# Kernel tuning notes

Measured on AMD Instinct MI355X. Metric: run time of the kernel, lower is better.

## Reference

```python
import jax, jax.numpy as jnp
import numpy as np

B, T, D, H = 131072, 30, 10, 20
EPS = 1e-5


def setup_inputs() -> dict:
    key = jax.random.key(0)
    ks = jax.random.split(key, 8)
    rn = lambda k, s: (jax.random.normal(k, s, dtype=jnp.float32) * 0.1)
    return {
        "x": jax.random.normal(ks[0], (B, T, D), dtype=jnp.float32),
        "g0": jnp.ones((T, 2 * D), jnp.float32),
        "be0": jnp.zeros((T, 2 * D), jnp.float32),
        "W1": rn(ks[1], (T, H, 2 * D)),
        "b1": rn(ks[2], (T, H)),
        "g1": jnp.ones((T, H), jnp.float32),
        "be1": jnp.zeros((T, H), jnp.float32),
        "W2": rn(ks[3], (T, H, H)),
        "b2": rn(ks[4], (T, H)),
        "g2": jnp.ones((T, H), jnp.float32),
        "be2": jnp.zeros((T, H), jnp.float32),
        "W3": rn(ks[5], (T, D, H)),
        "b3": rn(ks[6], (T, D)),
    }


def _bn(x, g, b):
    # training-mode BatchNorm1d: batch stats, biased variance, eps=1e-5
    mu = x.mean(0)
    var = ((x - mu) ** 2).mean(0)
    return (x - mu) * jax.lax.rsqrt(var + EPS) * g + b


def _forward(x, g0, be0, W1, b1, g1, be1, W2, b2, g2, be2, W3, b3):
    xs = jnp.swapaxes(x, 0, 1)  # [T, B, D] time-major

    def step(prev, ps):
        xt, g0t, be0t, W1t, b1t, g1t, be1t, W2t, b2t, g2t, be2t, W3t, b3t = ps
        h = jnp.concatenate([xt, prev], axis=1)      # [B, 2D] recurrent concat
        h = _bn(h, g0t, be0t)
        h = jax.nn.relu(_bn(h @ W1t.T + b1t, g1t, be1t))  # [B, H]
        h = jax.nn.relu(_bn(h @ W2t.T + b2t, g2t, be2t))  # [B, H]
        out = h @ W3t.T + b3t                              # [B, D]
        return out, out

    init = jnp.zeros((x.shape[0], D), dtype=x.dtype)
    _, outs = jax.lax.scan(step, init, (xs, g0, be0, W1, b1, g1, be1, W2, b2, g2, be2, W3, b3))
    return jnp.swapaxes(outs, 0, 1)  # [B, T, D]


def reference(x, g0, be0, W1, b1, g1, be1, W2, b2, g2, be2, W3, b3):
    return _forward(x, g0, be0, W1, b1, g1, be1, W2, b2, g2, be2, W3, b3)
```

## Files before the change

### kernel.cpp

```cpp
#include <hip/hip_runtime.h>

static constexpr int   BATCH = 131072;
static constexpr int   TS    = 30;
static constexpr int   DD    = 10;
static constexpr int   HH    = 20;
static constexpr float EPSV  = 1e-5f;
static constexpr float INV_B = 1.0f / (float)BATCH;

static constexpr int NBLK = 256;
static constexpr int NTHR = 256;
static constexpr int RPT  = 2;
static constexpr int TT   = NBLK * NTHR;
static constexpr int NS   = 8;
static constexpr int GRPS = 8;
static constexpr int GSZ  = NBLK / GRPS;
static constexpr int NVA  = 230;
static constexpr int NVB  = 40;
static constexpr int STRA = NVA * NS;
static constexpr int STRB = NVB * NS;
static constexpr int CTRW = 160;

__device__ __forceinline__ int tri(int k, int l) {
    return k * (41 - k) / 2 + (l - k);
}

template <int CTRL>
__device__ __forceinline__ float dpp_add(float v) {
    int x = __builtin_amdgcn_update_dpp(0, __float_as_int(v), CTRL, 0xF, 0xF, true);
    return v + __int_as_float(x);
}

__device__ __forceinline__ float rowsum16(float v) {
    v = dpp_add<0x111>(v);
    v = dpp_add<0x112>(v);
    v = dpp_add<0x114>(v);
    v = dpp_add<0x118>(v);
    return v;
}

__device__ __forceinline__ float aloadf(const float* p) {
    return __hip_atomic_load(p, __ATOMIC_RELAXED, __HIP_MEMORY_SCOPE_AGENT);
}

__device__ __forceinline__ void gbar(unsigned* __restrict__ base, int tid, int grp8) {
    __syncthreads();
    if (tid == 0) {
        if (__hip_atomic_fetch_add(base + grp8 * 16, 1u, __ATOMIC_RELAXED,
                                   __HIP_MEMORY_SCOPE_AGENT) == (unsigned)(GSZ - 1))
            __hip_atomic_fetch_add(base + 128, 1u, __ATOMIC_RELAXED,
                                   __HIP_MEMORY_SCOPE_AGENT);
        while (__hip_atomic_load(base + 128, __ATOMIC_RELAXED,
                                 __HIP_MEMORY_SCOPE_AGENT) < (unsigned)GRPS)
            __builtin_amdgcn_s_sleep(1);
    }
    __syncthreads();
}

__global__ void __launch_bounds__(NTHR)
k_init(const float* __restrict__ x, float* __restrict__ prevg, float* __restrict__ redA)
{
    __shared__ float lred[16 * NVA];
    const int tid     = threadIdx.x;
    const int grp     = tid >> 4;
    const bool lane15 = (tid & 15) == 15;
    const int gt      = blockIdx.x * NTHR + tid;

    float xv[RPT][DD];
#pragma unroll
    for (int r = 0; r < RPT; ++r) {
        const float2* px = reinterpret_cast<const float2*>(x + (size_t)(gt + r * TT) * TS * DD);
#pragma unroll
        for (int i = 0; i < 5; ++i) { float2 v = px[i]; xv[r][2 * i] = v.x; xv[r][2 * i + 1] = v.y; }
    }
#pragma unroll
    for (int r = 0; r < RPT; ++r)
#pragma unroll
        for (int d = 0; d < DD; ++d) prevg[(size_t)d * BATCH + gt + r * TT] = 0.0f;

#define H0A(i) ((i) < DD ? xv[0][i] : 0.0f)
#define H0B(i) ((i) < DD ? xv[1][i] : 0.0f)
    {
        int v = 0;
#pragma unroll
        for (int k = 0; k < 2 * DD; ++k) {
#pragma unroll
            for (int l = k; l < 2 * DD; ++l) {
                float p = fmaf(H0A(k), H0A(l), H0B(k) * H0B(l));
                float r = rowsum16(p);
                if (lane15) lred[grp * NVA + v] = r;
                ++v;
            }
        }
#pragma unroll
        for (int k = 0; k < 2 * DD; ++k) {
            float r = rowsum16(H0A(k) + H0B(k));
            if (lane15) lred[grp * NVA + 210 + k] = r;
        }
    }
#undef H0A
#undef H0B
    __syncthreads();
    if (tid < NVA) {
        float acc = 0.0f;
#pragma unroll
        for (int g = 0; g < 16; ++g) acc += lred[g * NVA + tid];
        atomicAdd(redA + tid * NS + (blockIdx.x & (NS - 1)), acc);
    }
}

template <bool LAST>
__global__ void __launch_bounds__(NTHR)
k_step(const float* __restrict__ x, float* __restrict__ prevg, float* __restrict__ outg,
       const float* __restrict__ W1, const float* __restrict__ W2,
       const float* __restrict__ W3, const float* __restrict__ b3,
       const float* __restrict__ g0, const float* __restrict__ be0,
       const float* __restrict__ g1, const float* __restrict__ be1,
       const float* __restrict__ g2, const float* __restrict__ be2,
       float* __restrict__ redA, float* __restrict__ redB,
       unsigned* __restrict__ ctr, int t)
{
    __shared__ float lred[16 * NVA];
    __shared__ float sM[230], sMu[20], sCov[400], sU[400], sP[400];
    __shared__ float sW1[400], sW2[400], sW3[200], sB3[10];
    __shared__ float sA0[20], sC0[20], sA1[20], sC1[20], sA2[20], sC2[20];

    const int tid     = threadIdx.x;
    const int grp     = tid >> 4;
    const bool lane15 = (tid & 15) == 15;
    const int slot    = blockIdx.x & (NS - 1);
    const int grp8    = blockIdx.x & (GRPS - 1);
    const int gt      = blockIdx.x * NTHR + tid;

    float xv[RPT][DD], pv[RPT][DD], xn[RPT][DD];
#pragma unroll
    for (int r = 0; r < RPT; ++r) {
        const float2* px = reinterpret_cast<const float2*>(x + (size_t)(gt + r * TT) * TS * DD + t * DD);
#pragma unroll
        for (int i = 0; i < 5; ++i) { float2 v = px[i]; xv[r][2 * i] = v.x; xv[r][2 * i + 1] = v.y; }
    }
#pragma unroll
    for (int r = 0; r < RPT; ++r)
#pragma unroll
        for (int d = 0; d < DD; ++d) pv[r][d] = prevg[(size_t)d * BATCH + gt + r * TT];
    if constexpr (!LAST) {
#pragma unroll
        for (int r = 0; r < RPT; ++r) {
            const float2* px = reinterpret_cast<const float2*>(x + (size_t)(gt + r * TT) * TS * DD + (t + 1) * DD);
#pragma unroll
            for (int i = 0; i < 5; ++i) { float2 v = px[i]; xn[r][2 * i] = v.x; xn[r][2 * i + 1] = v.y; }
        }
    }

    for (int i = tid; i < 400; i += NTHR) { sW1[i] = W1[t * 400 + i]; sW2[i] = W2[t * 400 + i]; }
    if (tid < 200) sW3[tid] = W3[t * 200 + tid];
    if (tid >= 200 && tid < 210) sB3[tid - 200] = b3[t * DD + (tid - 200)];

    if (tid < NVA) {
        const float* p = redA + (size_t)t * STRA + tid * NS;
        float s = 0.0f;
#pragma unroll
        for (int i = 0; i < NS; ++i) s += p[i];
        sM[tid] = s;
    }
    __syncthreads();

    if (tid < 20) {
        float mu  = sM[210 + tid] * INV_B;
        float var = fmaf(-mu, mu, sM[tri(tid, tid)] * INV_B);
        float a   = g0[t * 20 + tid] * rsqrtf(var + EPSV);
        sA0[tid] = a;
        sC0[tid] = fmaf(-mu, a, be0[t * 20 + tid]);
        sMu[tid] = mu;
    }
    __syncthreads();

    for (int i = tid; i < 400; i += NTHR) {
        int k = i / 20, l = i % 20;
        int a = k < l ? k : l, b = k < l ? l : k;
        sCov[i] = fmaf(-sMu[k], sMu[l], sM[tri(a, b)] * INV_B);
        sU[i]   = sW1[i] * sA0[l];
    }
    __syncthreads();

    for (int i = tid; i < 400; i += NTHR) {
        int j = i / 20, k = i % 20;
        float acc = 0.0f;
#pragma unroll
        for (int l = 0; l < 20; ++l)
            acc = fmaf(sCov[k * 20 + l], sU[j * 20 + l], acc);
        sP[i] = acc * sU[i];
    }
    __syncthreads();

    if (tid < 20) {
        float var1 = 0.0f, m1 = 0.0f;
#pragma unroll
        for (int k = 0; k < 20; ++k) {
            var1 += sP[tid * 20 + k];
            m1    = fmaf(sU[tid * 20 + k], sMu[k], m1);
            m1    = fmaf(sW1[tid * 20 + k], sC0[k], m1);
        }
        float a1 = g1[t * 20 + tid] * rsqrtf(var1 + EPSV);
        sA1[tid] = a1;
        sC1[tid] = fmaf(-m1, a1, be1[t * 20 + tid]);
    }
    __syncthreads();

    float y2[RPT][HH];
#pragma unroll
    for (int r = 0; r < RPT; ++r) {
        float hn[20];
#pragma unroll
        for (int k = 0; k < 10; ++k) hn[k]      = fmaf(xv[r][k], sA0[k],      sC0[k]);
#pragma unroll
        for (int k = 0; k < 10; ++k) hn[10 + k] = fmaf(pv[r][k], sA0[10 + k], sC0[10 + k]);

        float h1[20];
#pragma unroll
        for (int j = 0; j < 20; ++j) {
            float y = 0.0f;
#pragma unroll
            for (int k = 0; k < 20; ++k) y = fmaf(sW1[j * 20 + k], hn[k], y);
            h1[j] = fmaxf(fmaf(y, sA1[j], sC1[j]), 0.0f);
        }
#pragma unroll
        for (int j = 0; j < 20; ++j) {
            float y = 0.0f;
#pragma unroll
            for (int k = 0; k < 20; ++k) y = fmaf(sW2[j * 20 + k], h1[k], y);
            y2[r][j] = y;
        }
    }

#pragma unroll
    for (int j = 0; j < 20; ++j) {
        float r = rowsum16(y2[0][j] + y2[1][j]);
        if (lane15) lred[grp * NVA + j] = r;
    }
#pragma unroll
    for (int j = 0; j < 20; ++j) {
        float r = rowsum16(fmaf(y2[0][j], y2[0][j], y2[1][j] * y2[1][j]));
        if (lane15) lred[grp * NVA + 20 + j] = r;
    }
    __syncthreads();
    if (tid < NVB) {
        float acc = 0.0f;
#pragma unroll
        for (int g = 0; g < 16; ++g) acc += lred[g * NVA + tid];
        atomicAdd(redB + (size_t)t * STRB + tid * NS + slot, acc);
    }

    gbar(ctr + (size_t)t * CTRW, tid, grp8);

    if (tid < NVB) {
        const float* p = redB + (size_t)t * STRB + tid * NS;
        float s = 0.0f;
#pragma unroll
        for (int i = 0; i < NS; ++i) s += aloadf(p + i);
        sM[tid] = s;
    }
    __syncthreads();
    if (tid < 20) {
        float m   = sM[tid] * INV_B;
        float var = fmaf(-m, m, sM[20 + tid] * INV_B);
        float a   = g2[t * 20 + tid] * rsqrtf(var + EPSV);
        sA2[tid] = a;
        sC2[tid] = fmaf(-m, a, be2[t * 20 + tid]);
    }
    __syncthreads();

    float ov[RPT][DD];
#pragma unroll
    for (int r = 0; r < RPT; ++r) {
        float h2[20];
#pragma unroll
        for (int j = 0; j < 20; ++j)
            h2[j] = fmaxf(fmaf(y2[r][j], sA2[j], sC2[j]), 0.0f);
#pragma unroll
        for (int d = 0; d < DD; ++d) {
            float a = sB3[d];
#pragma unroll
            for (int j = 0; j < 20; ++j)
                a = fmaf(sW3[d * 20 + j], h2[j], a);
            ov[r][d] = a;
        }
        float2* po = reinterpret_cast<float2*>(outg + (size_t)(gt + r * TT) * TS * DD + t * DD);
#pragma unroll
        for (int i = 0; i < 5; ++i) po[i] = make_float2(ov[r][2 * i], ov[r][2 * i + 1]);
#pragma unroll
        for (int d = 0; d < DD; ++d) prevg[(size_t)d * BATCH + gt + r * TT] = ov[r][d];
    }

    if constexpr (!LAST) {
#define H0A(i) ((i) < DD ? xn[0][i] : ov[0][(i) - DD])
#define H0B(i) ((i) < DD ? xn[1][i] : ov[1][(i) - DD])
        {
            int v = 0;
#pragma unroll
            for (int k = 0; k < 2 * DD; ++k) {
#pragma unroll
                for (int l = k; l < 2 * DD; ++l) {
                    float p = fmaf(H0A(k), H0A(l), H0B(k) * H0B(l));
                    float r = rowsum16(p);
                    if (lane15) lred[grp * NVA + v] = r;
                    ++v;
                }
            }
#pragma unroll
            for (int k = 0; k < 2 * DD; ++k) {
                float r = rowsum16(H0A(k) + H0B(k));
                if (lane15) lred[grp * NVA + 210 + k] = r;
            }
        }
#undef H0A
#undef H0B
        __syncthreads();
        if (tid < NVA) {
            float acc = 0.0f;
#pragma unroll
            for (int g = 0; g < 16; ++g) acc += lred[g * NVA + tid];
            atomicAdd(redA + (size_t)(t + 1) * STRA + tid * NS + slot, acc);
        }
    }
}

extern "C" void kernel_launch(void* const* d_in, const int* in_sizes, int n_in,
                              void* d_out, int out_size, void* d_ws, size_t ws_size,
                              hipStream_t stream) {
    const float* x   = (const float*)d_in[0];
    const float* g0  = (const float*)d_in[1];
    const float* be0 = (const float*)d_in[2];
    const float* W1  = (const float*)d_in[3];
    const float* b1  = (const float*)d_in[4];   (void)b1;
    const float* g1  = (const float*)d_in[5];
    const float* be1 = (const float*)d_in[6];
    const float* W2  = (const float*)d_in[7];
    const float* b2  = (const float*)d_in[8];   (void)b2;
    const float* g2  = (const float*)d_in[9];
    const float* be2 = (const float*)d_in[10];
    const float* W3  = (const float*)d_in[11];
    const float* b3  = (const float*)d_in[12];
    float* out = (float*)d_out;

    const size_t redA_f = (size_t)TS * STRA;
    const size_t redB_f = (size_t)TS * STRB;
    const size_t ctr_u  = (size_t)TS * CTRW;
    float*    redA  = (float*)d_ws;
    float*    redB  = redA + redA_f;
    unsigned* ctr   = (unsigned*)(redB + redB_f);
    float*    prevg = (float*)(ctr + ctr_u);

    hipMemsetAsync(d_ws, 0, (redA_f + redB_f) * 4 + ctr_u * 4, stream);

    k_init<<<NBLK, NTHR, 0, stream>>>(x, prevg, redA);

    for (int t = 0; t < TS; ++t) {
        if (t + 1 < TS)
            k_step<false><<<NBLK, NTHR, 0, stream>>>(x, prevg, out, W1, W2, W3, b3,
                                                     g0, be0, g1, be1, g2, be2,
                                                     redA, redB, ctr, t);
        else
            k_step<true><<<NBLK, NTHR, 0, stream>>>(x, prevg, out, W1, W2, W3, b3,
                                                    g0, be0, g1, be1, g2, be2,
                                                    redA, redB, ctr, t);
    }
}
```

Measured before the change: 1.338 ms.

## Fuse all timesteps into one persistent kernel with grid barriers

Replaces the init kernel plus thirty per-step launches with a single persistent kernel that loops over timesteps. Software grid barriers on per-phase counters stand in for kernel boundaries. The recurrent state now stays in registers instead of round-tripping through a global prevg buffer. This removes launch gaps and global traffic for the state, but relies on all 256 blocks being co-resident and adds spin-wait barrier latency.

```diff
diff --git a/kernel.cpp b/kernel.cpp
--- a/kernel.cpp
+++ b/kernel.cpp
@@ -19,6 +19,7 @@
 static constexpr int STRA = NVA * NS;
 static constexpr int STRB = NVB * NS;
 static constexpr int CTRW = 160;
+static constexpr int NPH  = 2 * TS + 1;
 
 __device__ __forceinline__ int tri(int k, int l) {
     return k * (41 - k) / 2 + (l - k);
@@ -57,67 +58,14 @@
 }
 
 __global__ void __launch_bounds__(NTHR)
-k_init(const float* __restrict__ x, float* __restrict__ prevg, float* __restrict__ redA)
-{
-    __shared__ float lred[16 * NVA];
-    const int tid     = threadIdx.x;
-    const int grp     = tid >> 4;
-    const bool lane15 = (tid & 15) == 15;
-    const int gt      = blockIdx.x * NTHR + tid;
-
-    float xv[RPT][DD];
-#pragma unroll
-    for (int r = 0; r < RPT; ++r) {
-        const float2* px = reinterpret_cast<const float2*>(x + (size_t)(gt + r * TT) * TS * DD);
-#pragma unroll
-        for (int i = 0; i < 5; ++i) { float2 v = px[i]; xv[r][2 * i] = v.x; xv[r][2 * i + 1] = v.y; }
-    }
-#pragma unroll
-    for (int r = 0; r < RPT; ++r)
-#pragma unroll
-        for (int d = 0; d < DD; ++d) prevg[(size_t)d * BATCH + gt + r * TT] = 0.0f;
-
-#define H0A(i) ((i) < DD ? xv[0][i] : 0.0f)
-#define H0B(i) ((i) < DD ? xv[1][i] : 0.0f)
-    {
-        int v = 0;
-#pragma unroll
-        for (int k = 0; k < 2 * DD; ++k) {
-#pragma unroll
-            for (int l = k; l < 2 * DD; ++l) {
-                float p = fmaf(H0A(k), H0A(l), H0B(k) * H0B(l));
-                float r = rowsum16(p);
-                if (lane15) lred[grp * NVA + v] = r;
-                ++v;
-            }
-        }
-#pragma unroll
-        for (int k = 0; k < 2 * DD; ++k) {
-            float r = rowsum16(H0A(k) + H0B(k));
-            if (lane15) lred[grp * NVA + 210 + k] = r;
-        }
-    }
-#undef H0A
-#undef H0B
-    __syncthreads();
-    if (tid < NVA) {
-        float acc = 0.0f;
-#pragma unroll
-        for (int g = 0; g < 16; ++g) acc += lred[g * NVA + tid];
-        atomicAdd(redA + tid * NS + (blockIdx.x & (NS - 1)), acc);
-    }
-}
-
-template <bool LAST>
-__global__ void __launch_bounds__(NTHR)
-k_step(const float* __restrict__ x, float* __restrict__ prevg, float* __restrict__ outg,
-       const float* __restrict__ W1, const float* __restrict__ W2,
-       const float* __restrict__ W3, const float* __restrict__ b3,
-       const float* __restrict__ g0, const float* __restrict__ be0,
-       const float* __restrict__ g1, const float* __restrict__ be1,
-       const float* __restrict__ g2, const float* __restrict__ be2,
-       float* __restrict__ redA, float* __restrict__ redB,
-       unsigned* __restrict__ ctr, int t)
+rnn_all(const float* __restrict__ x, float* __restrict__ outg,
+        const float* __restrict__ W1, const float* __restrict__ W2,
+        const float* __restrict__ W3, const float* __restrict__ b3,
+        const float* __restrict__ g0, const float* __restrict__ be0,
+        const float* __restrict__ g1, const float* __restrict__ be1,
+        const float* __restrict__ g2, const float* __restrict__ be2,
+        float* __restrict__ redA, float* __restrict__ redB,
+        unsigned* __restrict__ ctr)
 {
     __shared__ float lred[16 * NVA];
     __shared__ float sM[230], sMu[20], sCov[400], sU[400], sP[400];
@@ -131,195 +79,238 @@
     const int grp8    = blockIdx.x & (GRPS - 1);
     const int gt      = blockIdx.x * NTHR + tid;
 
-    float xv[RPT][DD], pv[RPT][DD], xn[RPT][DD];
+    float pv[RPT][DD];
+#pragma unroll
+    for (int r = 0; r < RPT; ++r)
+#pragma unroll
+        for (int d = 0; d < DD; ++d) pv[r][d] = 0.0f;
+
+    float xv[RPT][DD];
 #pragma unroll
     for (int r = 0; r < RPT; ++r) {
-        const float2* px = reinterpret_cast<const float2*>(x + (size_t)(gt + r * TT) * TS * DD + t * DD);
+        const float2* px = reinterpret_cast<const float2*>(x + (size_t)(gt + r * TT) * TS * DD);
 #pragma unroll
         for (int i = 0; i < 5; ++i) { float2 v = px[i]; xv[r][2 * i] = v.x; xv[r][2 * i + 1] = v.y; }
     }
-#pragma unroll
-    for (int r = 0; r < RPT; ++r)
-#pragma unroll
-        for (int d = 0; d < DD; ++d) pv[r][d] = prevg[(size_t)d * BATCH + gt + r * TT];
-    if constexpr (!LAST) {
+
+#define H0A(i) ((i) < DD ? xv[0][i] : 0.0f)
+#define H0B(i) ((i) < DD ? xv[1][i] : 0.0f)
+    {
+        int v = 0;
+#pragma unroll
+        for (int k = 0; k < 2 * DD; ++k) {
+#pragma unroll
+            for (int l = k; l < 2 * DD; ++l) {
+                float p = fmaf(H0A(k), H0A(l), H0B(k) * H0B(l));
+                float r = rowsum16(p);
+                if (lane15) lred[grp * NVA + v] = r;
+                ++v;
+            }
+        }
+#pragma unroll
+        for (int k = 0; k < 2 * DD; ++k) {
+            float r = rowsum16(H0A(k) + H0B(k));
+            if (lane15) lred[grp * NVA + 210 + k] = r;
+        }
+    }
+#undef H0A
+#undef H0B
+    __syncthreads();
+    if (tid < NVA) {
+        float acc = 0.0f;
+#pragma unroll
+        for (int g = 0; g < 16; ++g) acc += lred[g * NVA + tid];
+        atomicAdd(redA + tid * NS + slot, acc);
+    }
+    gbar(ctr + (size_t)(2 * TS) * CTRW, tid, grp8);
+
+    for (int t = 0; t < TS; ++t) {
+        for (int i = tid; i < 400; i += NTHR) { sW1[i] = W1[t * 400 + i]; sW2[i] = W2[t * 400 + i]; }
+        if (tid < 200) sW3[tid] = W3[t * 200 + tid];
+        if (tid >= 200 && tid < 210) sB3[tid - 200] = b3[t * DD + (tid - 200)];
+
+        float xn[RPT][DD];
+        if (t + 1 < TS) {
+#pragma unroll
+            for (int r = 0; r < RPT; ++r) {
+                const float2* px = reinterpret_cast<const float2*>(x + (size_t)(gt + r * TT) * TS * DD + (t + 1) * DD);
+#pragma unroll
+                for (int i = 0; i < 5; ++i) { float2 v = px[i]; xn[r][2 * i] = v.x; xn[r][2 * i + 1] = v.y; }
+            }
+        }
+
+        if (tid < NVA) {
+            const float* p = redA + (size_t)t * STRA + tid * NS;
+            float s = 0.0f;
+#pragma unroll
+            for (int i = 0; i < NS; ++i) s += aloadf(p + i);
+            sM[tid] = s;
+        }
+        __syncthreads();
+
+        if (tid < 20) {
+            float mu  = sM[210 + tid] * INV_B;
+            float var = fmaf(-mu, mu, sM[tri(tid, tid)] * INV_B);
+            float a   = g0[t * 20 + tid] * rsqrtf(var + EPSV);
+            sA0[tid] = a;
+            sC0[tid] = fmaf(-mu, a, be0[t * 20 + tid]);
+            sMu[tid] = mu;
+        }
+        __syncthreads();
+
+        for (int i = tid; i < 400; i += NTHR) {
+            int k = i / 20, l = i % 20;
+            int a = k < l ? k : l, b = k < l ? l : k;
+            sCov[i] = fmaf(-sMu[k], sMu[l], sM[tri(a, b)] * INV_B);
+            sU[i]   = sW1[i] * sA0[l];
+        }
+        __syncthreads();
+
+        for (int i = tid; i < 400; i += NTHR) {
+            int j = i / 20, k = i % 20;
+            float acc = 0.0f;
+#pragma unroll
+            for (int l = 0; l < 20; ++l)
+                acc = fmaf(sCov[k * 20 + l], sU[j * 20 + l], acc);
+            sP[i] = acc * sU[i];
+        }
+        __syncthreads();
+
+        if (tid < 20) {
+            float var1 = 0.0f, m1 = 0.0f;
+#pragma unroll
+            for (int k = 0; k < 20; ++k) {
+                var1 += sP[tid * 20 + k];
+                m1    = fmaf(sU[tid * 20 + k], sMu[k], m1);
+                m1    = fmaf(sW1[tid * 20 + k], sC0[k], m1);
+            }
+            float a1 = g1[t * 20 + tid] * rsqrtf(var1 + EPSV);
+            sA1[tid] = a1;
+            sC1[tid] = fmaf(-m1, a1, be1[t * 20 + tid]);
+        }
+        __syncthreads();
+
+        float y2[RPT][HH];
 #pragma unroll
         for (int r = 0; r < RPT; ++r) {
-            const float2* px = reinterpret_cast<const float2*>(x + (size_t)(gt + r * TT) * TS * DD + (t + 1) * DD);
-#pragma unroll
-            for (int i = 0; i < 5; ++i) { float2 v = px[i]; xn[r][2 * i] = v.x; xn[r][2 * i + 1] = v.y; }
-        }
-    }
-
-    for (int i = tid; i < 400; i += NTHR) { sW1[i] = W1[t * 400 + i]; sW2[i] = W2[t * 400 + i]; }
-    if (tid < 200) sW3[tid] = W3[t * 200 + tid];
-    if (tid >= 200 && tid < 210) sB3[tid - 200] = b3[t * DD + (tid - 200)];
-
-    if (tid < NVA) {
-        const float* p = redA + (size_t)t * STRA + tid * NS;
-        float s = 0.0f;
-#pragma unroll
-        for (int i = 0; i < NS; ++i) s += p[i];
-        sM[tid] = s;
-    }
-    __syncthreads();
-
-    if (tid < 20) {
-        float mu  = sM[210 + tid] * INV_B;
-        float var = fmaf(-mu, mu, sM[tri(tid, tid)] * INV_B);
-        float a   = g0[t * 20 + tid] * rsqrtf(var + EPSV);
-        sA0[tid] = a;
-        sC0[tid] = fmaf(-mu, a, be0[t * 20 + tid]);
-        sMu[tid] = mu;
-    }
-    __syncthreads();
-
-    for (int i = tid; i < 400; i += NTHR) {
-        int k = i / 20, l = i % 20;
-        int a = k < l ? k : l, b = k < l ? l : k;
-        sCov[i] = fmaf(-sMu[k], sMu[l], sM[tri(a, b)] * INV_B);
-        sU[i]   = sW1[i] * sA0[l];
-    }
-    __syncthreads();
-
-    for (int i = tid; i < 400; i += NTHR) {
-        int j = i / 20, k = i % 20;
-        float acc = 0.0f;
-#pragma unroll
-        for (int l = 0; l < 20; ++l)
-            acc = fmaf(sCov[k * 20 + l], sU[j * 20 + l], acc);
-        sP[i] = acc * sU[i];
-    }
-    __syncthreads();
-
-    if (tid < 20) {
-        float var1 = 0.0f, m1 = 0.0f;
-#pragma unroll
-        for (int k = 0; k < 20; ++k) {
-            var1 += sP[tid * 20 + k];
-            m1    = fmaf(sU[tid * 20 + k], sMu[k], m1);
-            m1    = fmaf(sW1[tid * 20 + k], sC0[k], m1);
-        }
-        float a1 = g1[t * 20 + tid] * rsqrtf(var1 + EPSV);
-        sA1[tid] = a1;
-        sC1[tid] = fmaf(-m1, a1, be1[t * 20 + tid]);
-    }
-    __syncthreads();
-
-    float y2[RPT][HH];
-#pragma unroll
-    for (int r = 0; r < RPT; ++r) {
-        float hn[20];
-#pragma unroll
-        for (int k = 0; k < 10; ++k) hn[k]      = fmaf(xv[r][k], sA0[k],      sC0[k]);
-#pragma unroll
-        for (int k = 0; k < 10; ++k) hn[10 + k] = fmaf(pv[r][k], sA0[10 + k], sC0[10 + k]);
-
-        float h1[20];
+            float hn[20];
+#pragma unroll
+            for (int k = 0; k < 10; ++k) hn[k]      = fmaf(xv[r][k], sA0[k],      sC0[k]);
+#pragma unroll
+            for (int k = 0; k < 10; ++k) hn[10 + k] = fmaf(pv[r][k], sA0[10 + k], sC0[10 + k]);
+
+            float h1[20];
+#pragma unroll
+            for (int j = 0; j < 20; ++j) {
+                float y = 0.0f;
+#pragma unroll
+                for (int k = 0; k < 20; ++k) y = fmaf(sW1[j * 20 + k], hn[k], y);
+                h1[j] = fmaxf(fmaf(y, sA1[j], sC1[j]), 0.0f);
+            }
+#pragma unroll
+            for (int j = 0; j < 20; ++j) {
+                float y = 0.0f;
+#pragma unroll
+                for (int k = 0; k < 20; ++k) y = fmaf(sW2[j * 20 + k], h1[k], y);
+                y2[r][j] = y;
+            }
+        }
+
 #pragma unroll
         for (int j = 0; j < 20; ++j) {
-            float y = 0.0f;
-#pragma unroll
-            for (int k = 0; k < 20; ++k) y = fmaf(sW1[j * 20 + k], hn[k], y);
-            h1[j] = fmaxf(fmaf(y, sA1[j], sC1[j]), 0.0f);
+            float r = rowsum16(y2[0][j] + y2[1][j]);
+            if (lane15) lred[grp * NVA + j] = r;
         }
 #pragma unroll
         for (int j = 0; j < 20; ++j) {
-            float y = 0.0f;
-#pragma unroll
-            for (int k = 0; k < 20; ++k) y = fmaf(sW2[j * 20 + k], h1[k], y);
-            y2[r][j] = y;
-        }
-    }
-
-#pragma unroll
-    for (int j = 0; j < 20; ++j) {
-        float r = rowsum16(y2[0][j] + y2[1][j]);
-        if (lane15) lred[grp * NVA + j] = r;
-    }
-#pragma unroll
-    for (int j = 0; j < 20; ++j) {
-        float r = rowsum16(fmaf(y2[0][j], y2[0][j], y2[1][j] * y2[1][j]));
-        if (lane15) lred[grp * NVA + 20 + j] = r;
-    }
-    __syncthreads();
-    if (tid < NVB) {
-        float acc = 0.0f;
-#pragma unroll
-        for (int g = 0; g < 16; ++g) acc += lred[g * NVA + tid];
-        atomicAdd(redB + (size_t)t * STRB + tid * NS + slot, acc);
-    }
-
-    gbar(ctr + (size_t)t * CTRW, tid, grp8);
-
-    if (tid < NVB) {
-        const float* p = redB + (size_t)t * STRB + tid * NS;
-        float s = 0.0f;
-#pragma unroll
-        for (int i = 0; i < NS; ++i) s += aloadf(p + i);
-        sM[tid] = s;
-    }
-    __syncthreads();
-    if (tid < 20) {
-        float m   = sM[tid] * INV_B;
-        float var = fmaf(-m, m, sM[20 + tid] * INV_B);
-        float a   = g2[t * 20 + tid] * rsqrtf(var + EPSV);
-        sA2[tid] = a;
-        sC2[tid] = fmaf(-m, a, be2[t * 20 + tid]);
-    }
-    __syncthreads();
-
-    float ov[RPT][DD];
-#pragma unroll
-    for (int r = 0; r < RPT; ++r) {
-        float h2[20];
-#pragma unroll
-        for (int j = 0; j < 20; ++j)
-            h2[j] = fmaxf(fmaf(y2[r][j], sA2[j], sC2[j]), 0.0f);
-#pragma unroll
-        for (int d = 0; d < DD; ++d) {
-            float a = sB3[d];
+            float r = rowsum16(fmaf(y2[0][j], y2[0][j], y2[1][j] * y2[1][j]));
+            if (lane15) lred[grp * NVA + 20 + j] = r;
+        }
+        __syncthreads();
+        if (tid < NVB) {
+            float acc = 0.0f;
+#pragma unroll
+            for (int g = 0; g < 16; ++g) acc += lred[g * NVA + tid];
+            atomicAdd(redB + (size_t)t * STRB + tid * NS + slot, acc);
+        }
+
+        gbar(ctr + (size_t)(2 * t) * CTRW, tid, grp8);
+
+        if (tid < NVB) {
+            const float* p = redB + (size_t)t * STRB + tid * NS;
+            float s = 0.0f;
+#pragma unroll
+            for (int i = 0; i < NS; ++i) s += aloadf(p + i);
+            sM[tid] = s;
+        }
+        __syncthreads();
+        if (tid < 20) {
+            float m   = sM[tid] * INV_B;
+            float var = fmaf(-m, m, sM[20 + tid] * INV_B);
+            float a   = g2[t * 20 + tid] * rsqrtf(var + EPSV);
+            sA2[tid] = a;
+            sC2[tid] = fmaf(-m, a, be2[t * 20 + tid]);
+        }
+        __syncthreads();
+
+        float ov[RPT][DD];
+#pragma unroll
+        for (int r = 0; r < RPT; ++r) {
+            float h2[20];
 #pragma unroll
             for (int j = 0; j < 20; ++j)
-                a = fmaf(sW3[d * 20 + j], h2[j], a);
-            ov[r][d] = a;
-        }
-        float2* po = reinterpret_cast<float2*>(outg + (size_t)(gt + r * TT) * TS * DD + t * DD);
-#pragma unroll
-        for (int i = 0; i < 5; ++i) po[i] = make_float2(ov[r][2 * i], ov[r][2 * i + 1]);
-#pragma unroll
-        for (int d = 0; d < DD; ++d) prevg[(size_t)d * BATCH + gt + r * TT] = ov[r][d];
-    }
-
-    if constexpr (!LAST) {
+                h2[j] = fmaxf(fmaf(y2[r][j], sA2[j], sC2[j]), 0.0f);
+#pragma unroll
+            for (int d = 0; d < DD; ++d) {
+                float a = sB3[d];
+#pragma unroll
+                for (int j = 0; j < 20; ++j)
+                    a = fmaf(sW3[d * 20 + j], h2[j], a);
+                ov[r][d] = a;
+            }
+            float2* po = reinterpret_cast<float2*>(outg + (size_t)(gt + r * TT) * TS * DD + t * DD);
+#pragma unroll
+            for (int i = 0; i < 5; ++i) po[i] = make_float2(ov[r][2 * i], ov[r][2 * i + 1]);
+#pragma unroll
+            for (int d = 0; d < DD; ++d) pv[r][d] = ov[r][d];
+        }
+
+        if (t + 1 < TS) {
 #define H0A(i) ((i) < DD ? xn[0][i] : ov[0][(i) - DD])
 #define H0B(i) ((i) < DD ? xn[1][i] : ov[1][(i) - DD])
-        {
-            int v = 0;
-#pragma unroll
-            for (int k = 0; k < 2 * DD; ++k) {
-#pragma unroll
-                for (int l = k; l < 2 * DD; ++l) {
-                    float p = fmaf(H0A(k), H0A(l), H0B(k) * H0B(l));
-                    float r = rowsum16(p);
-                    if (lane15) lred[grp * NVA + v] = r;
-                    ++v;
+            {
+                int v = 0;
+#pragma unroll
+                for (int k = 0; k < 2 * DD; ++k) {
+#pragma unroll
+                    for (int l = k; l < 2 * DD; ++l) {
+                        float p = fmaf(H0A(k), H0A(l), H0B(k) * H0B(l));
+                        float r = rowsum16(p);
+                        if (lane15) lred[grp * NVA + v] = r;
+                        ++v;
+                    }
                 }
-            }
-#pragma unroll
-            for (int k = 0; k < 2 * DD; ++k) {
-                float r = rowsum16(H0A(k) + H0B(k));
-                if (lane15) lred[grp * NVA + 210 + k] = r;
-            }
-        }
+#pragma unroll
+                for (int k = 0; k < 2 * DD; ++k) {
+                    float r = rowsum16(H0A(k) + H0B(k));
+                    if (lane15) lred[grp * NVA + 210 + k] = r;
+                }
+            }
 #undef H0A
 #undef H0B
-        __syncthreads();
-        if (tid < NVA) {
-            float acc = 0.0f;
-#pragma unroll
-            for (int g = 0; g < 16; ++g) acc += lred[g * NVA + tid];
-            atomicAdd(redA + (size_t)(t + 1) * STRA + tid * NS + slot, acc);
+            __syncthreads();
+            if (tid < NVA) {
+                float acc = 0.0f;
+#pragma unroll
+                for (int g = 0; g < 16; ++g) acc += lred[g * NVA + tid];
+                atomicAdd(redA + (size_t)(t + 1) * STRA + tid * NS + slot, acc);
+            }
+            gbar(ctr + (size_t)(2 * t + 1) * CTRW, tid, grp8);
+
+#pragma unroll
+            for (int r = 0; r < RPT; ++r)
+#pragma unroll
+                for (int d = 0; d < DD; ++d) xv[r][d] = xn[r][d];
         }
     }
 }
@@ -344,24 +335,14 @@
 
     const size_t redA_f = (size_t)TS * STRA;
     const size_t redB_f = (size_t)TS * STRB;
-    const size_t ctr_u  = (size_t)TS * CTRW;
+    const size_t ctr_u  = (size_t)NPH * CTRW;
     float*    redA  = (float*)d_ws;
     float*    redB  = redA + redA_f;
     unsigned* ctr   = (unsigned*)(redB + redB_f);
-    float*    prevg = (float*)(ctr + ctr_u);
 
     hipMemsetAsync(d_ws, 0, (redA_f + redB_f) * 4 + ctr_u * 4, stream);
 
-    k_init<<<NBLK, NTHR, 0, stream>>>(x, prevg, redA);
-
-    for (int t = 0; t < TS; ++t) {
-        if (t + 1 < TS)
-            k_step<false><<<NBLK, NTHR, 0, stream>>>(x, prevg, out, W1, W2, W3, b3,
-                                                     g0, be0, g1, be1, g2, be2,
-                                                     redA, redB, ctr, t);
-        else
-            k_step<true><<<NBLK, NTHR, 0, stream>>>(x, prevg, out, W1, W2, W3, b3,
-                                                    g0, be0, g1, be1, g2, be2,
-                                                    redA, redB, ctr, t);
-    }
-}
+    rnn_all<<<NBLK, NTHR, 0, stream>>>(x, out, W1, W2, W3, b3,
+                                       g0, be0, g1, be1, g2, be2,
+                                       redA, redB, ctr);
+}
```

After: 1.299 ms. 2.9% less time.
